# Performance work log

Hardware: AMD Instinct MI355X
Metric: run time of the kernel (lower is better)

The kernel has to match this reference:

```python
import jax, jax.numpy as jnp
import numpy as np

HEADS = 8
DIM_HEAD = 64
BN_EPS = 1e-5

def setup_inputs() -> dict:
    key = jax.random.key(0)
    ks = jax.random.split(key, 6)
    B, N, D = 8, 1024, 512
    inner = HEADS * DIM_HEAD  # 512
    return {
        "x": jax.random.normal(ks[0], (B, N, D), dtype=jnp.float32),
        "w_qkv": jax.random.normal(ks[1], (D, 3 * inner), dtype=jnp.float32) * (D ** -0.5),
        "conv_w": jax.random.normal(ks[2], (HEADS, HEADS), dtype=jnp.float32) * (HEADS ** -0.5),
        "conv_b": jax.random.normal(ks[3], (HEADS,), dtype=jnp.float32) * 0.02,
        "bn_gamma": jnp.ones((HEADS,), dtype=jnp.float32),
        "bn_beta": jnp.zeros((HEADS,), dtype=jnp.float32),
        "w_out": jax.random.normal(ks[4], (inner, D), dtype=jnp.float32) * (inner ** -0.5),
        "b_out": jnp.zeros((D,), dtype=jnp.float32),
    }

def reference(x, w_qkv, conv_w, conv_b, bn_gamma, bn_beta, w_out, b_out):
    B, N, D = x.shape
    H, dh = HEADS, DIM_HEAD
    scale = dh ** -0.5
    qkv = x @ w_qkv  # [B, N, 3*H*dh]
    q, k, v = jnp.split(qkv, 3, axis=-1)
    # b n (h d) -> b h n d
    q = q.reshape(B, N, H, dh).transpose(0, 2, 1, 3)
    k = k.reshape(B, N, H, dh).transpose(0, 2, 1, 3)
    v = v.reshape(B, N, H, dh).transpose(0, 2, 1, 3)
    attn = jnp.einsum('bhnd,bhmd->bhnm', q, k) * scale
    attn = jax.nn.softmax(attn, axis=-1)
    # 1x1 conv across heads (channels = heads)
    attn = jnp.einsum('gh,bhnm->bgnm', conv_w, attn) + conv_b[None, :, None, None]
    # BatchNorm2d in training mode: batch stats over (B, N, N) per head, biased variance
    mean = attn.mean(axis=(0, 2, 3), keepdims=True)
    var = attn.var(axis=(0, 2, 3), keepdims=True)
    attn = (attn - mean) * jax.lax.rsqrt(var + BN_EPS)
    attn = attn * bn_gamma[None, :, None, None] + bn_beta[None, :, None, None]
    # reatten_scale = 1.0 (transform_scale=False)
    out = jnp.einsum('bhnm,bhmd->bhnd', attn, v)
    out = out.transpose(0, 2, 1, 3).reshape(B, N, H * dh)  # b h n d -> b n (h d)
    return out @ w_out + b_out
```

## Files before the change

### kernel.cpp

```cpp
#include <hip/hip_runtime.h>
#include <math.h>


#define Bz 8
#define Nn 1024
#define Dd 512
#define Hh 8
#define DH 64
#define INNER 512
#define QW 1536
#define SCALE 0.125f
#define BN_EPS 1e-5f

typedef _Float16 __f16;
typedef __f16 f16x8 __attribute__((ext_vector_type(8)));
typedef float f32x4 __attribute__((ext_vector_type(4)));

#define MFMA16(a, b, c) __builtin_amdgcn_mfma_f32_16x16x32_f16((a), (b), (c), 0, 0, 0)

__device__ __forceinline__ unsigned short f2h(float f) {
  union { __f16 h; unsigned short s; } v;
  v.h = (__f16)f;
  return v.s;
}
__device__ __forceinline__ float h2f(unsigned short s) {
  union { unsigned short s; __f16 h; } v;
  v.s = s;
  return (float)v.h;
}

#define WB_XB 0u
#define WB_QKV 8388608u
#define WB_O1 0u
#define WB_VT 33554432u
#define WB_SG 41943040u
#define WB_O1BF WB_SG
#define WB_WQT 176160768u
#define WB_WOT 177733632u
#define WB_RSUM 178257920u
#define WB_VSUM 178520064u
#define WB_STATS 178536448u
#define WB_AC 178536512u

__global__ __launch_bounds__(256) void k_xbf(const float* __restrict__ X,
                                             unsigned short* __restrict__ XB) {
  const size_t i = ((size_t)blockIdx.x * 256 + threadIdx.x) * 8;
  float4 f0 = *(const float4*)(X + i);
  float4 f1 = *(const float4*)(X + i + 4);
  unsigned short o[8] = {f2h(f0.x), f2h(f0.y), f2h(f0.z), f2h(f0.w),
                         f2h(f1.x), f2h(f1.y), f2h(f1.z), f2h(f1.w)};
  *(uint4*)(XB + i) = *(uint4*)o;
}

__global__ __launch_bounds__(256) void k_transpose(const float* __restrict__ src,
                                                   unsigned short* __restrict__ dst,
                                                   int R, int C) {
  __shared__ float tile[32][33];
  const int tc = blockIdx.x * 32, tr = blockIdx.y * 32;
  const int lx = threadIdx.x & 31, ly = threadIdx.x >> 5;
#pragma unroll
  for (int i = 0; i < 32; i += 8)
    tile[ly + i][lx] = src[(size_t)(tr + ly + i) * C + tc + lx];
  __syncthreads();
#pragma unroll
  for (int i = 0; i < 32; i += 8)
    dst[(size_t)(tc + ly + i) * R + tr + lx] = f2h(tile[lx][ly + i]);
}

__global__ __launch_bounds__(256) void k_qkv(const unsigned short* __restrict__ XB,
                                             const unsigned short* __restrict__ WQT,
                                             unsigned short* __restrict__ qkv,
                                             unsigned short* __restrict__ vT) {
  extern __shared__ char smem[];
  unsigned short(*sA)[40] = (unsigned short(*)[40])smem;
  unsigned short(*sB)[40] = (unsigned short(*)[40])(smem + 128 * 40 * 2);
  unsigned short* sEp = (unsigned short*)smem;
  const int t = threadIdx.x;
  const int col0 = blockIdx.x * 128;
  const int row0 = blockIdx.y * 128;
  const bool isqk = (col0 < 2 * INNER);
  const int l = t & 63, w = t >> 6;
  const int wm = (w & 1) * 64, wn = (w >> 1) * 64;
  const int lm = l & 15, lq = l >> 4;
  const int srow = t >> 1, skc = (t & 1) * 16;
  f32x4 acc[4][4] = {};
  for (int k0 = 0; k0 < Dd; k0 += 32) {
    {
      const unsigned short* src = XB + (size_t)(row0 + srow) * Dd + k0 + skc;
      *(uint4*)&sA[srow][skc] = *(const uint4*)src;
      *(uint4*)&sA[srow][skc + 8] = *(const uint4*)(src + 8);
    }
    {
      const unsigned short* srcB = WQT + (size_t)(col0 + srow) * Dd + k0 + skc;
      *(uint4*)&sB[srow][skc] = *(const uint4*)srcB;
      *(uint4*)&sB[srow][skc + 8] = *(const uint4*)(srcB + 8);
    }
    __syncthreads();
    f16x8 af[4], bfr[4];
#pragma unroll
    for (int i = 0; i < 4; i++) af[i] = *(const f16x8*)&sA[wm + 16 * i + lm][lq * 8];
#pragma unroll
    for (int j = 0; j < 4; j++) bfr[j] = *(const f16x8*)&sB[wn + 16 * j + lm][lq * 8];
    if (isqk) {
#pragma unroll
      for (int i = 0; i < 4; i++)
#pragma unroll
        for (int j = 0; j < 4; j++) acc[i][j] = MFMA16(bfr[i], af[j], acc[i][j]);
    } else {
#pragma unroll
      for (int i = 0; i < 4; i++)
#pragma unroll
        for (int j = 0; j < 4; j++) acc[i][j] = MFMA16(af[i], bfr[j], acc[i][j]);
    }
    __syncthreads();
  }
  if (isqk) {
#pragma unroll
    for (int jc = 0; jc < 4; jc++)
#pragma unroll
      for (int ir = 0; ir < 4; ir++) {
        unsigned short us[4];
#pragma unroll
        for (int r = 0; r < 4; r++) us[r] = f2h(acc[jc][ir][r]);
        *(uint2*)&sEp[(wm + 16 * ir + lm) * 136 + wn + 16 * jc + 4 * lq] = *(uint2*)us;
      }
    __syncthreads();
    const int row = t >> 1, half = t & 1;
    const unsigned short* src = &sEp[row * 136 + half * 64];
    unsigned short* dst = qkv + (size_t)(row0 + row) * QW + col0 + half * 64;
#pragma unroll
    for (int c = 0; c < 8; c++) *(uint4*)(dst + c * 8) = *(const uint4*)(src + c * 8);
  } else {
#pragma unroll
    for (int ir = 0; ir < 4; ir++)
#pragma unroll
      for (int jc = 0; jc < 4; jc++) {
        unsigned short us[4];
#pragma unroll
        for (int r = 0; r < 4; r++) us[r] = f2h(acc[ir][jc][r]);
        *(uint2*)&sEp[(wn + 16 * jc + lm) * 136 + wm + 16 * ir + 4 * lq] = *(uint2*)us;
      }
    __syncthreads();
    const int row = t >> 1, half = t & 1;
    const int gd = col0 - 2 * INNER + row;
    const int bq = row0 >> 10, mseq0 = row0 & 1023;
    const unsigned short* src = &sEp[row * 136 + half * 64];
    unsigned short* dst =
        vT + (((size_t)(bq * Hh + (gd >> 6)) * DH + (gd & 63)) << 10) + mseq0 + half * 64;
#pragma unroll
    for (int c = 0; c < 8; c++) *(uint4*)(dst + c * 8) = *(const uint4*)(src + c * 8);
  }
}

__global__ __launch_bounds__(256) void k_vsum(const unsigned short* __restrict__ vT,
                                              float* __restrict__ vsum) {
  const int bg = blockIdx.x;
  const int d = threadIdx.x >> 2, qq = threadIdx.x & 3;
  __shared__ float red[64][4];
  const unsigned short* p = vT + ((size_t)bg * DH + d) * Nn + qq * 256;
  float s = 0.f;
  for (int m = 0; m < 256; m += 4) {
    uint2 rr = *(const uint2*)(p + m);
    s += h2f((unsigned short)(rr.x & 0xffff)) + h2f((unsigned short)(rr.x >> 16)) +
         h2f((unsigned short)(rr.y & 0xffff)) + h2f((unsigned short)(rr.y >> 16));
  }
  red[d][qq] = s;
  __syncthreads();
  if (threadIdx.x < 64)
    vsum[(size_t)bg * DH + threadIdx.x] =
        red[threadIdx.x][0] + red[threadIdx.x][1] + red[threadIdx.x][2] + red[threadIdx.x][3];
}

__global__ __launch_bounds__(512, 2) void k_sgen(const unsigned short* __restrict__ qkv,
                                                 unsigned short* __restrict__ Sg,
                                                 float* __restrict__ rsum) {
  __shared__ unsigned short sK[8 * 32 * 72];
  __shared__ unsigned short sT[32 * 264];
  const int b = blockIdx.x;
  const int n0 = blockIdx.y * 32;
  const int mh = blockIdx.z;
  const int t = threadIdx.x;
  const int w = t >> 6, l = t & 63;
  const int lm = l & 15, lq = l >> 4;
  f16x8 qf[2][2];
#pragma unroll
  for (int i = 0; i < 2; i++) {
    const unsigned short* qp =
        qkv + (size_t)(b * Nn + n0 + 16 * i + lm) * QW + w * DH + lq * 8;
    qf[i][0] = *(const f16x8*)qp;
    qf[i][1] = *(const f16x8*)(qp + 32);
  }
  float psum[2] = {0.f, 0.f};
  for (int it = 0; it < 16; it++) {
    const int m0 = mh * 512 + it * 32;
    {
#pragma unroll
      for (int s = 0; s < 4; s++) {
        const int c = t + s * 512;
        const int hh = c >> 8, mm = (c >> 3) & 31, qq = c & 7;
        *(uint4*)&sK[(hh * 32 + mm) * 72 + qq * 8] = *(const uint4*)(
            qkv + (size_t)(b * Nn + m0 + mm) * QW + INNER + hh * DH + qq * 8);
      }
    }
    __syncthreads();
    f32x4 lac[2][2] = {};
#pragma unroll
    for (int jm = 0; jm < 2; jm++) {
      f16x8 ka0 = *(const f16x8*)&sK[(w * 32 + 16 * jm + lm) * 72 + lq * 8];
      f16x8 ka1 = *(const f16x8*)&sK[(w * 32 + 16 * jm + lm) * 72 + 32 + lq * 8];
#pragma unroll
      for (int i = 0; i < 2; i++) {
        lac[i][jm] = MFMA16(ka0, qf[i][0], lac[i][jm]);
        lac[i][jm] = MFMA16(ka1, qf[i][1], lac[i][jm]);
      }
    }
#pragma unroll
    for (int i = 0; i < 2; i++)
#pragma unroll
      for (int jm = 0; jm < 2; jm++)
#pragma unroll
        for (int r = 0; r < 4; r++) {
          float e = __expf(lac[i][jm][r] * SCALE);
          psum[i] += e;
          sT[(16 * i + lm) * 264 + (16 * jm + 4 * lq + r) * 8 + w] = f2h(e);
        }
    __syncthreads();
    {
      const int row = t >> 4, ck = t & 15;
      unsigned short* dst =
          Sg + (((size_t)(b * Nn + n0 + row) << 10) + m0) * 8 + ck * 16;
      const unsigned short* src = &sT[row * 264 + ck * 16];
      *(uint4*)dst = *(const uint4*)src;
      *(uint4*)(dst + 8) = *(const uint4*)(src + 8);
    }
  }
#pragma unroll
  for (int i = 0; i < 2; i++) {
    psum[i] += __shfl_xor(psum[i], 16);
    psum[i] += __shfl_xor(psum[i], 32);
  }
  if (lq == 0) {
    atomicAdd(&rsum[(size_t)(b * Hh + w) * Nn + n0 + lm], psum[0]);
    atomicAdd(&rsum[(size_t)(b * Hh + w) * Nn + n0 + 16 + lm], psum[1]);
  }
}

__global__ __launch_bounds__(512, 2) void k_mixsv(const unsigned short* __restrict__ Sg,
                                                  const unsigned short* __restrict__ vT,
                                                  const float* __restrict__ rsum,
                                                  const float* __restrict__ conv_w,
                                                  float* __restrict__ O1,
                                                  float* __restrict__ stats) {
  __shared__ unsigned short sU[8][16][68];
  __shared__ float sRed[8][16];
  const int b = blockIdx.x;
  const int n0 = blockIdx.y * 16;
  const int t = threadIdx.x;
  const int w = t >> 6, l = t & 63;
  const int lm = l & 15, lq = l >> 4;
  const int mxn = t >> 5, mxm = (t & 31) * 2;
  float cw[64];
#pragma unroll
  for (int i = 0; i < 64; i++) cw[i] = conv_w[i];
  float rv[8];
#pragma unroll
  for (int h = 0; h < 8; h++) rv[h] = 1.0f / rsum[(size_t)(b * Hh + h) * Nn + n0 + mxn];
  const unsigned short* sNp = Sg + ((size_t)(b * Nn + n0 + mxn) << 13);
  f32x4 oacc[4] = {};
  float su[8] = {}, su2[8] = {};
  uint4 c0, c1;
  {
    const unsigned short* p = sNp + (mxm << 3);
    c0 = *(const uint4*)p;
    c1 = *(const uint4*)(p + 8);
  }
  for (int it = 0; it < 16; it++) {
    uint4 nx0, nx1;
    if (it < 15) {
      const unsigned short* p = sNp + ((size_t)((it + 1) * 64 + mxm) << 3);
      nx0 = *(const uint4*)p;
      nx1 = *(const uint4*)(p + 8);
    }
    {
      const unsigned* pe = (const unsigned*)&c0;
      const unsigned* po = (const unsigned*)&c1;
      float sx[8], sy[8];
#pragma unroll
      for (int hp = 0; hp < 4; hp++) {
        sx[2 * hp] = h2f((unsigned short)(pe[hp] & 0xffff)) * rv[2 * hp];
        sx[2 * hp + 1] = h2f((unsigned short)(pe[hp] >> 16)) * rv[2 * hp + 1];
        sy[2 * hp] = h2f((unsigned short)(po[hp] & 0xffff)) * rv[2 * hp];
        sy[2 * hp + 1] = h2f((unsigned short)(po[hp] >> 16)) * rv[2 * hp + 1];
      }
#pragma unroll
      for (int g = 0; g < 8; g++) {
        float u0 = 0.f, u1 = 0.f;
#pragma unroll
        for (int h = 0; h < 8; h++) {
          u0 += cw[g * 8 + h] * sx[h];
          u1 += cw[g * 8 + h] * sy[h];
        }
        su[g] += u0 + u1;
        su2[g] += u0 * u0 + u1 * u1;
        *(unsigned*)&sU[g][mxn][mxm] = (unsigned)f2h(u0) | ((unsigned)f2h(u1) << 16);
      }
    }
    __syncthreads();
    {
      f16x8 uf0 = *(const f16x8*)&sU[w][lm][lq * 8];
      f16x8 uf1 = *(const f16x8*)&sU[w][lm][32 + lq * 8];
#pragma unroll
      for (int j = 0; j < 4; j++) {
        const unsigned short* vp =
            vT + (((size_t)(b * Hh + w) * DH + 16 * j + lm) << 10) + it * 64 + lq * 8;
        f16x8 v0 = *(const f16x8*)vp;
        f16x8 v1 = *(const f16x8*)(vp + 32);
        oacc[j] = MFMA16(uf0, v0, oacc[j]);
        oacc[j] = MFMA16(uf1, v1, oacc[j]);
      }
    }
    __syncthreads();
    if (it < 15) {
      c0 = nx0;
      c1 = nx1;
    }
  }
#pragma unroll
  for (int j = 0; j < 4; j++)
#pragma unroll
    for (int r = 0; r < 4; r++)
      O1[((size_t)(b * Hh + w) * Nn + n0 + lq * 4 + r) * DH + 16 * j + lm] = oacc[j][r];
#pragma unroll
  for (int g = 0; g < 8; g++) {
    float a = su[g], q = su2[g];
    for (int off = 32; off; off >>= 1) {
      a += __shfl_down(a, off);
      q += __shfl_down(q, off);
    }
    if (l == 0) {
      sRed[w][g] = a;
      sRed[w][8 + g] = q;
    }
  }
  __syncthreads();
  if (t < 16) {
    float s = 0.f;
#pragma unroll
    for (int ww = 0; ww < 8; ww++) s += sRed[ww][t];
    atomicAdd(&stats[t], s);
  }
}

__global__ void k_alpha(const float* __restrict__ stats, const float* __restrict__ bn_gamma,
                        const float* __restrict__ bn_beta, float* __restrict__ ac) {
  const int g = threadIdx.x;
  if (g < 8) {
    const float cnt = (float)Bz * (float)Nn * (float)Nn;
    float Eu = stats[g] / cnt;
    float Eu2 = stats[8 + g] / cnt;
    float inv = rsqrtf(Eu2 - Eu * Eu + BN_EPS);
    float alpha = bn_gamma[g] * inv;
    ac[g] = alpha;
    ac[8 + g] = bn_beta[g] - Eu * alpha;
  }
}

__global__ __launch_bounds__(256) void k_o1aff(const float* __restrict__ O1,
                                               const float* __restrict__ vsum,
                                               const float* __restrict__ ac,
                                               unsigned short* __restrict__ O1BF) {
  const size_t i4 = ((size_t)blockIdx.x * 256 + threadIdx.x) * 4;
  const int bg = (int)(i4 >> 16);
  const int g = bg & 7;
  const int d = (int)(i4 & 63);
  float4 a = *(const float4*)(O1 + i4);
  float4 v = *(const float4*)(vsum + (size_t)bg * DH + d);
  const float al = ac[g], cc = ac[8 + g];
  unsigned short o[4] = {f2h(al * a.x + cc * v.x), f2h(al * a.y + cc * v.y),
                         f2h(al * a.z + cc * v.z), f2h(al * a.w + cc * v.w)};
  *(uint2*)(O1BF + i4) = *(uint2*)o;
}

__global__ __launch_bounds__(256) void k_out(const unsigned short* __restrict__ O1BF,
                                             const unsigned short* __restrict__ WOT,
                                             const float* __restrict__ bout,
                                             float* __restrict__ out) {
  __shared__ unsigned short sA[128][40];
  __shared__ unsigned short sB[128][40];
  const int t = threadIdx.x;
  const int col0 = blockIdx.x * 128, row0 = blockIdx.y * 128;
  const int l = t & 63, w = t >> 6;
  const int wm = (w & 1) * 64, wn = (w >> 1) * 64;
  const int lm = l & 15, lq = l >> 4;
  const int srow = t >> 1, skc = (t & 1) * 16;
  const int b = row0 >> 10;
  const int nn = (row0 + srow) & 1023;
  f32x4 acc[4][4] = {};
  for (int k0 = 0; k0 < INNER; k0 += 32) {
    {
      const int k = k0 + skc;
      const int g = k >> 6, dd = k & 63;
      const unsigned short* src = O1BF + ((size_t)(b * Hh + g) * Nn + nn) * DH + dd;
      *(uint4*)&sA[srow][skc] = *(const uint4*)src;
      *(uint4*)&sA[srow][skc + 8] = *(const uint4*)(src + 8);
    }
    {
      const unsigned short* srcB = WOT + (size_t)(col0 + srow) * INNER + k0 + skc;
      *(uint4*)&sB[srow][skc] = *(const uint4*)srcB;
      *(uint4*)&sB[srow][skc + 8] = *(const uint4*)(srcB + 8);
    }
    __syncthreads();
    f16x8 af[4], bfr[4];
#pragma unroll
    for (int i = 0; i < 4; i++) af[i] = *(const f16x8*)&sA[wm + 16 * i + lm][lq * 8];
#pragma unroll
    for (int j = 0; j < 4; j++) bfr[j] = *(const f16x8*)&sB[wn + 16 * j + lm][lq * 8];
#pragma unroll
    for (int i = 0; i < 4; i++)
#pragma unroll
      for (int j = 0; j < 4; j++) acc[i][j] = MFMA16(af[i], bfr[j], acc[i][j]);
    __syncthreads();
  }
#pragma unroll
  for (int j = 0; j < 4; j++) {
    const int col = col0 + wn + 16 * j + lm;
    const float bo = bout[col];
#pragma unroll
    for (int i = 0; i < 4; i++) {
      const int rbase = row0 + wm + 16 * i + lq * 4;
#pragma unroll
      for (int r = 0; r < 4; r++) out[(size_t)(rbase + r) * Dd + col] = acc[i][j][r] + bo;
    }
  }
}

extern "C" void kernel_launch(void* const* d_in, const int* in_sizes, int n_in,
                              void* d_out, int out_size, void* d_ws, size_t ws_size,
                              hipStream_t stream) {
  const float* x = (const float*)d_in[0];
  const float* w_qkv = (const float*)d_in[1];
  const float* conv_w = (const float*)d_in[2];
  const float* bn_gamma = (const float*)d_in[4];
  const float* bn_beta = (const float*)d_in[5];
  const float* w_out = (const float*)d_in[6];
  const float* b_out = (const float*)d_in[7];
  char* ws = (char*)d_ws;
  unsigned short* XB = (unsigned short*)(ws + WB_XB);
  unsigned short* QKV = (unsigned short*)(ws + WB_QKV);
  unsigned short* VT = (unsigned short*)(ws + WB_VT);
  unsigned short* SG = (unsigned short*)(ws + WB_SG);
  unsigned short* WQT = (unsigned short*)(ws + WB_WQT);
  unsigned short* WOT = (unsigned short*)(ws + WB_WOT);
  float* O1 = (float*)(ws + WB_O1);
  unsigned short* O1BF = (unsigned short*)(ws + WB_O1BF);
  float* RSUM = (float*)(ws + WB_RSUM);
  float* VSUM = (float*)(ws + WB_VSUM);
  float* STATS = (float*)(ws + WB_STATS);
  float* AC = (float*)(ws + WB_AC);

  hipMemsetAsync(STATS, 0, 64, stream);
  hipMemsetAsync(RSUM, 0, 262144, stream);
  k_xbf<<<2048, 256, 0, stream>>>(x, XB);
  k_transpose<<<dim3(48, 16), 256, 0, stream>>>(w_qkv, WQT, 512, 1536);
  k_transpose<<<dim3(16, 16), 256, 0, stream>>>(w_out, WOT, 512, 512);
  k_qkv<<<dim3(12, 64), 256, 34816, stream>>>(XB, WQT, QKV, VT);
  k_vsum<<<64, 256, 0, stream>>>(VT, VSUM);
  k_sgen<<<dim3(8, 32, 2), 512, 0, stream>>>(QKV, SG, RSUM);
  k_mixsv<<<dim3(8, 64), 512, 0, stream>>>(SG, VT, RSUM, conv_w, O1, STATS);
  k_alpha<<<1, 64, 0, stream>>>(STATS, bn_gamma, bn_beta, AC);
  k_o1aff<<<4096, 256, 0, stream>>>(O1, VSUM, AC, O1BF);
  k_out<<<dim3(4, 64), 256, 0, stream>>>(O1BF, WOT, b_out, (float*)d_out);
}
```

Before: 271.7 us.

## Double-buffer mix LDS tile, use packed fp16 scaling, derive BN mean analytically

The head-mix kernel now double-buffers its shared-memory tile, so one barrier per iteration is removed, and V fragments are loaded before the barrier. Softmax normalisation is done with packed fp16 multiplies and the result is converted with pkrtz. The BN mean is computed from the conv weight row sums (softmax rows sum to 1, conv bias ignored as before), which drops the running-sum accumulation. The risks are extra fp16 rounding in the scaling step and extra LDS use.

```diff
diff --git a/kernel.cpp b/kernel.cpp
--- a/kernel.cpp
+++ b/kernel.cpp
@@ -14,6 +14,8 @@
 
 typedef _Float16 __f16;
 typedef __f16 f16x8 __attribute__((ext_vector_type(8)));
+typedef __f16 f16x2 __attribute__((ext_vector_type(2)));
+typedef __fp16 fp16x2 __attribute__((ext_vector_type(2)));
 typedef float f32x4 __attribute__((ext_vector_type(4)));
 
 #define MFMA16(a, b, c) __builtin_amdgcn_mfma_f32_16x16x32_f16((a), (b), (c), 0, 0, 0)
@@ -251,8 +253,8 @@
                                                   const float* __restrict__ conv_w,
                                                   float* __restrict__ O1,
                                                   float* __restrict__ stats) {
-  __shared__ unsigned short sU[8][16][68];
-  __shared__ float sRed[8][16];
+  __shared__ unsigned short sU[2][8][16][68];
+  __shared__ float sRed[8][8];
   const int b = blockIdx.x;
   const int n0 = blockIdx.y * 16;
   const int t = threadIdx.x;
@@ -262,68 +264,80 @@
   float cw[64];
 #pragma unroll
   for (int i = 0; i < 64; i++) cw[i] = conv_w[i];
-  float rv[8];
-#pragma unroll
-  for (int h = 0; h < 8; h++) rv[h] = 1.0f / rsum[(size_t)(b * Hh + h) * Nn + n0 + mxn];
+  f16x2 rvh2[4];
+#pragma unroll
+  for (int hp = 0; hp < 4; hp++) {
+    float r0 = 1.0f / rsum[(size_t)(b * Hh + 2 * hp) * Nn + n0 + mxn];
+    float r1 = 1.0f / rsum[(size_t)(b * Hh + 2 * hp + 1) * Nn + n0 + mxn];
+    f16x2 rr;
+    rr[0] = (__f16)r0;
+    rr[1] = (__f16)r1;
+    rvh2[hp] = rr;
+  }
   const unsigned short* sNp = Sg + ((size_t)(b * Nn + n0 + mxn) << 13);
   f32x4 oacc[4] = {};
-  float su[8] = {}, su2[8] = {};
+  float su2[8] = {};
   uint4 c0, c1;
   {
     const unsigned short* p = sNp + (mxm << 3);
     c0 = *(const uint4*)p;
     c1 = *(const uint4*)(p + 8);
   }
+  int p = 0;
   for (int it = 0; it < 16; it++) {
     uint4 nx0, nx1;
     if (it < 15) {
-      const unsigned short* p = sNp + ((size_t)((it + 1) * 64 + mxm) << 3);
-      nx0 = *(const uint4*)p;
-      nx1 = *(const uint4*)(p + 8);
-    }
-    {
-      const unsigned* pe = (const unsigned*)&c0;
-      const unsigned* po = (const unsigned*)&c1;
-      float sx[8], sy[8];
+      const unsigned short* pp = sNp + ((size_t)((it + 1) * 64 + mxm) << 3);
+      nx0 = *(const uint4*)pp;
+      nx1 = *(const uint4*)(pp + 8);
+    }
+    {
+      const f16x2* pe2 = (const f16x2*)&c0;
+      const f16x2* po2 = (const f16x2*)&c1;
+      f16x2 eh[4], oh[4];
 #pragma unroll
       for (int hp = 0; hp < 4; hp++) {
-        sx[2 * hp] = h2f((unsigned short)(pe[hp] & 0xffff)) * rv[2 * hp];
-        sx[2 * hp + 1] = h2f((unsigned short)(pe[hp] >> 16)) * rv[2 * hp + 1];
-        sy[2 * hp] = h2f((unsigned short)(po[hp] & 0xffff)) * rv[2 * hp];
-        sy[2 * hp + 1] = h2f((unsigned short)(po[hp] >> 16)) * rv[2 * hp + 1];
+        eh[hp] = pe2[hp] * rvh2[hp];
+        oh[hp] = po2[hp] * rvh2[hp];
       }
 #pragma unroll
       for (int g = 0; g < 8; g++) {
         float u0 = 0.f, u1 = 0.f;
 #pragma unroll
-        for (int h = 0; h < 8; h++) {
-          u0 += cw[g * 8 + h] * sx[h];
-          u1 += cw[g * 8 + h] * sy[h];
+        for (int hp = 0; hp < 4; hp++) {
+          u0 = fmaf((float)eh[hp][0], cw[g * 8 + 2 * hp], u0);
+          u0 = fmaf((float)eh[hp][1], cw[g * 8 + 2 * hp + 1], u0);
+          u1 = fmaf((float)oh[hp][0], cw[g * 8 + 2 * hp], u1);
+          u1 = fmaf((float)oh[hp][1], cw[g * 8 + 2 * hp + 1], u1);
         }
-        su[g] += u0 + u1;
-        su2[g] += u0 * u0 + u1 * u1;
-        *(unsigned*)&sU[g][mxn][mxm] = (unsigned)f2h(u0) | ((unsigned)f2h(u1) << 16);
-      }
-    }
-    __syncthreads();
-    {
-      f16x8 uf0 = *(const f16x8*)&sU[w][lm][lq * 8];
-      f16x8 uf1 = *(const f16x8*)&sU[w][lm][32 + lq * 8];
+        su2[g] = fmaf(u0, u0, fmaf(u1, u1, su2[g]));
+        fp16x2 pk = __builtin_amdgcn_cvt_pkrtz(u0, u1);
+        *(unsigned*)&sU[p][g][mxn][mxm] = *(unsigned*)&pk;
+      }
+    }
+    f16x8 va[4], vb[4];
+#pragma unroll
+    for (int j = 0; j < 4; j++) {
+      const unsigned short* vp =
+          vT + (((size_t)(b * Hh + w) * DH + 16 * j + lm) << 10) + it * 64 + lq * 8;
+      va[j] = *(const f16x8*)vp;
+      vb[j] = *(const f16x8*)(vp + 32);
+    }
+    __syncthreads();
+    {
+      f16x8 uf0 = *(const f16x8*)&sU[p][w][lm][lq * 8];
+      f16x8 uf1 = *(const f16x8*)&sU[p][w][lm][32 + lq * 8];
 #pragma unroll
       for (int j = 0; j < 4; j++) {
-        const unsigned short* vp =
-            vT + (((size_t)(b * Hh + w) * DH + 16 * j + lm) << 10) + it * 64 + lq * 8;
-        f16x8 v0 = *(const f16x8*)vp;
-        f16x8 v1 = *(const f16x8*)(vp + 32);
-        oacc[j] = MFMA16(uf0, v0, oacc[j]);
-        oacc[j] = MFMA16(uf1, v1, oacc[j]);
-      }
-    }
-    __syncthreads();
+        oacc[j] = MFMA16(uf0, va[j], oacc[j]);
+        oacc[j] = MFMA16(uf1, vb[j], oacc[j]);
+      }
+    }
     if (it < 15) {
       c0 = nx0;
       c1 = nx1;
     }
+    p ^= 1;
   }
 #pragma unroll
   for (int j = 0; j < 4; j++)
@@ -332,31 +346,29 @@
       O1[((size_t)(b * Hh + w) * Nn + n0 + lq * 4 + r) * DH + 16 * j + lm] = oacc[j][r];
 #pragma unroll
   for (int g = 0; g < 8; g++) {
-    float a = su[g], q = su2[g];
-    for (int off = 32; off; off >>= 1) {
-      a += __shfl_down(a, off);
-      q += __shfl_down(q, off);
-    }
-    if (l == 0) {
-      sRed[w][g] = a;
-      sRed[w][8 + g] = q;
-    }
+    float q = su2[g];
+    for (int off = 32; off; off >>= 1) q += __shfl_down(q, off);
+    if (l == 0) sRed[w][g] = q;
   }
   __syncthreads();
-  if (t < 16) {
+  if (t < 8) {
     float s = 0.f;
 #pragma unroll
     for (int ww = 0; ww < 8; ww++) s += sRed[ww][t];
-    atomicAdd(&stats[t], s);
-  }
-}
-
-__global__ void k_alpha(const float* __restrict__ stats, const float* __restrict__ bn_gamma,
+    atomicAdd(&stats[8 + t], s);
+  }
+}
+
+__global__ void k_alpha(const float* __restrict__ stats, const float* __restrict__ conv_w,
+                        const float* __restrict__ bn_gamma,
                         const float* __restrict__ bn_beta, float* __restrict__ ac) {
   const int g = threadIdx.x;
   if (g < 8) {
     const float cnt = (float)Bz * (float)Nn * (float)Nn;
-    float Eu = stats[g] / cnt;
+    float sc = 0.f;
+#pragma unroll
+    for (int h = 0; h < 8; h++) sc += conv_w[g * 8 + h];
+    float Eu = sc * (1.0f / (float)Nn);
     float Eu2 = stats[8 + g] / cnt;
     float inv = rsqrtf(Eu2 - Eu * Eu + BN_EPS);
     float alpha = bn_gamma[g] * inv;
@@ -467,7 +479,7 @@
   k_vsum<<<64, 256, 0, stream>>>(VT, VSUM);
   k_sgen<<<dim3(8, 32, 2), 512, 0, stream>>>(QKV, SG, RSUM);
   k_mixsv<<<dim3(8, 64), 512, 0, stream>>>(SG, VT, RSUM, conv_w, O1, STATS);
-  k_alpha<<<1, 64, 0, stream>>>(STATS, bn_gamma, bn_beta, AC);
+  k_alpha<<<1, 64, 0, stream>>>(STATS, conv_w, bn_gamma, bn_beta, AC);
   k_o1aff<<<4096, 256, 0, stream>>>(O1, VSUM, AC, O1BF);
   k_out<<<dim3(4, 64), 256, 0, stream>>>(O1BF, WOT, b_out, (float*)d_out);
 }
```

Result: no change. 273.4 us (+0.6%).

## Compute BN stats via head Gram matrix and apply conv after PV matmul

Applied to the files above, without the earlier changes.

The head-mixing 1x1 conv is moved from the attention matrix to after the per-head P·V products. Each warp now computes all 8 heads' S·V with MFMA and combines them with conv weights scaled by the inverse row sums. BatchNorm variance is computed from an 8x8 Gram matrix of normalized probabilities, contracted with conv_w in k_alpha. The mean is taken analytically from the row-sum-to-one property. The score tensor layout changes to per-head rows so the MFMA can read it directly. This removes the scalar per-element conv mixing and LDS staging, but multiplies MFMA work by 8 and adds redundant global re-reads of S for the Gram terms.

```diff
diff --git a/kernel.cpp b/kernel.cpp
--- a/kernel.cpp
+++ b/kernel.cpp
@@ -32,6 +32,7 @@
 #define WB_XB 0u
 #define WB_QKV 8388608u
 #define WB_O1 0u
+#define WB_CMAT 29360128u
 #define WB_VT 33554432u
 #define WB_SG 41943040u
 #define WB_O1BF WB_SG
@@ -39,7 +40,6 @@
 #define WB_WOT 177733632u
 #define WB_RSUM 178257920u
 #define WB_VSUM 178520064u
-#define WB_STATS 178536448u
 #define WB_AC 178536512u
 
 __global__ __launch_bounds__(256) void k_xbf(const float* __restrict__ X,
@@ -175,7 +175,7 @@
                                                  unsigned short* __restrict__ Sg,
                                                  float* __restrict__ rsum) {
   __shared__ unsigned short sK[8 * 32 * 72];
-  __shared__ unsigned short sT[32 * 264];
+  __shared__ unsigned short sT2[8][32][40];
   const int b = blockIdx.x;
   const int n0 = blockIdx.y * 32;
   const int mh = blockIdx.z;
@@ -217,22 +217,25 @@
 #pragma unroll
     for (int i = 0; i < 2; i++)
 #pragma unroll
-      for (int jm = 0; jm < 2; jm++)
+      for (int jm = 0; jm < 2; jm++) {
+        unsigned short us[4];
 #pragma unroll
         for (int r = 0; r < 4; r++) {
           float e = __expf(lac[i][jm][r] * SCALE);
           psum[i] += e;
-          sT[(16 * i + lm) * 264 + (16 * jm + 4 * lq + r) * 8 + w] = f2h(e);
+          us[r] = f2h(e);
         }
-    __syncthreads();
-    {
-      const int row = t >> 4, ck = t & 15;
+        *(uint2*)&sT2[w][16 * i + lm][16 * jm + 4 * lq] = *(uint2*)us;
+      }
+    {
+      const int row = l >> 1, half = l & 1;
+      const unsigned short* src = &sT2[w][row][half * 16];
       unsigned short* dst =
-          Sg + (((size_t)(b * Nn + n0 + row) << 10) + m0) * 8 + ck * 16;
-      const unsigned short* src = &sT[row * 264 + ck * 16];
+          Sg + ((size_t)(b * Hh + w) * Nn + n0 + row) * Nn + m0 + half * 16;
       *(uint4*)dst = *(const uint4*)src;
       *(uint4*)(dst + 8) = *(const uint4*)(src + 8);
     }
+    __syncthreads();
   }
 #pragma unroll
   for (int i = 0; i < 2; i++) {
@@ -250,114 +253,113 @@
                                                   const float* __restrict__ rsum,
                                                   const float* __restrict__ conv_w,
                                                   float* __restrict__ O1,
-                                                  float* __restrict__ stats) {
-  __shared__ unsigned short sU[8][16][68];
-  __shared__ float sRed[8][16];
+                                                  float* __restrict__ cmat) {
   const int b = blockIdx.x;
   const int n0 = blockIdx.y * 16;
   const int t = threadIdx.x;
   const int w = t >> 6, l = t & 63;
   const int lm = l & 15, lq = l >> 4;
-  const int mxn = t >> 5, mxm = (t & 31) * 2;
-  float cw[64];
-#pragma unroll
-  for (int i = 0; i < 64; i++) cw[i] = conv_w[i];
-  float rv[8];
-#pragma unroll
-  for (int h = 0; h < 8; h++) rv[h] = 1.0f / rsum[(size_t)(b * Hh + h) * Nn + n0 + mxn];
-  const unsigned short* sNp = Sg + ((size_t)(b * Nn + n0 + mxn) << 13);
-  f32x4 oacc[4] = {};
-  float su[8] = {}, su2[8] = {};
-  uint4 c0, c1;
+  const unsigned short* sb[8];
+#pragma unroll
+  for (int h = 0; h < 8; h++)
+    sb[h] = Sg + ((size_t)(b * Hh + h) * Nn + n0 + lm) * Nn + lq * 8;
+  const unsigned short* vbase = vT + (((size_t)(b * Hh + w) * DH + lm) << 10) + lq * 8;
+  f32x4 acc[8][4] = {};
+  float gam[8] = {0.f, 0.f, 0.f, 0.f, 0.f, 0.f, 0.f, 0.f};
+  for (int it = 0; it < 16; it++) {
+    const int m0 = it * 64;
+    f16x8 va[4], vb[4];
+#pragma unroll
+    for (int j = 0; j < 4; j++) {
+      va[j] = *(const f16x8*)(vbase + (j << 14) + m0);
+      vb[j] = *(const f16x8*)(vbase + (j << 14) + m0 + 32);
+    }
+#pragma unroll
+    for (int h = 0; h < 8; h++) {
+      f16x8 a0 = *(const f16x8*)(sb[h] + m0);
+      f16x8 a1 = *(const f16x8*)(sb[h] + m0 + 32);
+#pragma unroll
+      for (int j = 0; j < 4; j++) {
+        acc[h][j] = MFMA16(a0, va[j], acc[h][j]);
+        acc[h][j] = MFMA16(a1, vb[j], acc[h][j]);
+      }
+    }
+#pragma unroll
+    for (int h = 0; h < 8; h++) {
+      const int h2 = (w - h) & 7;
+      if (h2 >= h) {
+        f16x8 x0 = *(const f16x8*)(sb[h] + m0);
+        f16x8 x1 = *(const f16x8*)(sb[h] + m0 + 32);
+        f16x8 y0 = *(const f16x8*)(sb[h2] + m0);
+        f16x8 y1 = *(const f16x8*)(sb[h2] + m0 + 32);
+        float g = gam[h];
+#pragma unroll
+        for (int s = 0; s < 8; s++) {
+          g = fmaf((float)x0[s], (float)y0[s], g);
+          g = fmaf((float)x1[s], (float)y1[s], g);
+        }
+        gam[h] = g;
+      }
+    }
+  }
   {
-    const unsigned short* p = sNp + (mxm << 3);
-    c0 = *(const uint4*)p;
-    c1 = *(const uint4*)(p + 8);
-  }
-  for (int it = 0; it < 16; it++) {
-    uint4 nx0, nx1;
-    if (it < 15) {
-      const unsigned short* p = sNp + ((size_t)((it + 1) * 64 + mxm) << 3);
-      nx0 = *(const uint4*)p;
-      nx1 = *(const uint4*)(p + 8);
-    }
-    {
-      const unsigned* pe = (const unsigned*)&c0;
-      const unsigned* po = (const unsigned*)&c1;
-      float sx[8], sy[8];
-#pragma unroll
-      for (int hp = 0; hp < 4; hp++) {
-        sx[2 * hp] = h2f((unsigned short)(pe[hp] & 0xffff)) * rv[2 * hp];
-        sx[2 * hp + 1] = h2f((unsigned short)(pe[hp] >> 16)) * rv[2 * hp + 1];
-        sy[2 * hp] = h2f((unsigned short)(po[hp] & 0xffff)) * rv[2 * hp];
-        sy[2 * hp + 1] = h2f((unsigned short)(po[hp] >> 16)) * rv[2 * hp + 1];
-      }
-#pragma unroll
-      for (int g = 0; g < 8; g++) {
-        float u0 = 0.f, u1 = 0.f;
-#pragma unroll
-        for (int h = 0; h < 8; h++) {
-          u0 += cw[g * 8 + h] * sx[h];
-          u1 += cw[g * 8 + h] * sy[h];
-        }
-        su[g] += u0 + u1;
-        su2[g] += u0 * u0 + u1 * u1;
-        *(unsigned*)&sU[g][mxn][mxm] = (unsigned)f2h(u0) | ((unsigned)f2h(u1) << 16);
-      }
-    }
-    __syncthreads();
-    {
-      f16x8 uf0 = *(const f16x8*)&sU[w][lm][lq * 8];
-      f16x8 uf1 = *(const f16x8*)&sU[w][lm][32 + lq * 8];
-#pragma unroll
-      for (int j = 0; j < 4; j++) {
-        const unsigned short* vp =
-            vT + (((size_t)(b * Hh + w) * DH + 16 * j + lm) << 10) + it * 64 + lq * 8;
-        f16x8 v0 = *(const f16x8*)vp;
-        f16x8 v1 = *(const f16x8*)(vp + 32);
-        oacc[j] = MFMA16(uf0, v0, oacc[j]);
-        oacc[j] = MFMA16(uf1, v1, oacc[j]);
-      }
-    }
-    __syncthreads();
-    if (it < 15) {
-      c0 = nx0;
-      c1 = nx1;
-    }
+    float rvl[8];
+#pragma unroll
+    for (int h = 0; h < 8; h++)
+      rvl[h] = 1.0f / rsum[(size_t)(b * Hh + h) * Nn + n0 + lm];
+#pragma unroll
+    for (int h = 0; h < 8; h++) {
+      const int h2 = (w - h) & 7;
+      if (h2 >= h) {
+        float g = gam[h] * rvl[h] * rvl[h2];
+#pragma unroll
+        for (int off = 32; off; off >>= 1) g += __shfl_down(g, off);
+        if (l == 0) atomicAdd(&cmat[h * 8 + h2], g);
+      }
+    }
+  }
+  float cw8[8];
+#pragma unroll
+  for (int h = 0; h < 8; h++) cw8[h] = conv_w[w * 8 + h];
+  float sc[8][4];
+#pragma unroll
+  for (int h = 0; h < 8; h++) {
+    float4 rr = *(const float4*)&rsum[(size_t)(b * Hh + h) * Nn + n0 + lq * 4];
+    sc[h][0] = cw8[h] / rr.x;
+    sc[h][1] = cw8[h] / rr.y;
+    sc[h][2] = cw8[h] / rr.z;
+    sc[h][3] = cw8[h] / rr.w;
   }
 #pragma unroll
   for (int j = 0; j < 4; j++)
 #pragma unroll
-    for (int r = 0; r < 4; r++)
-      O1[((size_t)(b * Hh + w) * Nn + n0 + lq * 4 + r) * DH + 16 * j + lm] = oacc[j][r];
-#pragma unroll
-  for (int g = 0; g < 8; g++) {
-    float a = su[g], q = su2[g];
-    for (int off = 32; off; off >>= 1) {
-      a += __shfl_down(a, off);
-      q += __shfl_down(q, off);
-    }
-    if (l == 0) {
-      sRed[w][g] = a;
-      sRed[w][8 + g] = q;
-    }
-  }
-  __syncthreads();
-  if (t < 16) {
-    float s = 0.f;
-#pragma unroll
-    for (int ww = 0; ww < 8; ww++) s += sRed[ww][t];
-    atomicAdd(&stats[t], s);
-  }
-}
-
-__global__ void k_alpha(const float* __restrict__ stats, const float* __restrict__ bn_gamma,
+    for (int r = 0; r < 4; r++) {
+      float o = 0.f;
+#pragma unroll
+      for (int h = 0; h < 8; h++) o = fmaf(sc[h][r], acc[h][j][r], o);
+      O1[((size_t)(b * Hh + w) * Nn + n0 + lq * 4 + r) * DH + 16 * j + lm] = o;
+    }
+}
+
+__global__ void k_alpha(const float* __restrict__ cmat, const float* __restrict__ conv_w,
+                        const float* __restrict__ bn_gamma,
                         const float* __restrict__ bn_beta, float* __restrict__ ac) {
   const int g = threadIdx.x;
   if (g < 8) {
     const float cnt = (float)Bz * (float)Nn * (float)Nn;
-    float Eu = stats[g] / cnt;
-    float Eu2 = stats[8 + g] / cnt;
+    float scw = 0.f;
+#pragma unroll
+    for (int h = 0; h < 8; h++) scw += conv_w[g * 8 + h];
+    float Eu = scw * (1.0f / (float)Nn);
+    float Eu2 = 0.f;
+#pragma unroll
+    for (int h = 0; h < 8; h++)
+#pragma unroll
+      for (int h2 = h; h2 < 8; h2++) {
+        float mul = (h == h2) ? 1.f : 2.f;
+        Eu2 += mul * conv_w[g * 8 + h] * conv_w[g * 8 + h2] * cmat[h * 8 + h2];
+      }
+    Eu2 /= cnt;
     float inv = rsqrtf(Eu2 - Eu * Eu + BN_EPS);
     float alpha = bn_gamma[g] * inv;
     ac[g] = alpha;
@@ -455,10 +457,9 @@
   unsigned short* O1BF = (unsigned short*)(ws + WB_O1BF);
   float* RSUM = (float*)(ws + WB_RSUM);
   float* VSUM = (float*)(ws + WB_VSUM);
-  float* STATS = (float*)(ws + WB_STATS);
+  float* CMAT = (float*)(ws + WB_CMAT);
   float* AC = (float*)(ws + WB_AC);
 
-  hipMemsetAsync(STATS, 0, 64, stream);
   hipMemsetAsync(RSUM, 0, 262144, stream);
   k_xbf<<<2048, 256, 0, stream>>>(x, XB);
   k_transpose<<<dim3(48, 16), 256, 0, stream>>>(w_qkv, WQT, 512, 1536);
@@ -466,8 +467,9 @@
   k_qkv<<<dim3(12, 64), 256, 34816, stream>>>(XB, WQT, QKV, VT);
   k_vsum<<<64, 256, 0, stream>>>(VT, VSUM);
   k_sgen<<<dim3(8, 32, 2), 512, 0, stream>>>(QKV, SG, RSUM);
-  k_mixsv<<<dim3(8, 64), 512, 0, stream>>>(SG, VT, RSUM, conv_w, O1, STATS);
-  k_alpha<<<1, 64, 0, stream>>>(STATS, bn_gamma, bn_beta, AC);
+  hipMemsetAsync(CMAT, 0, 256, stream);
+  k_mixsv<<<dim3(8, 64), 512, 0, stream>>>(SG, VT, RSUM, conv_w, O1, CMAT);
+  k_alpha<<<1, 64, 0, stream>>>(CMAT, conv_w, bn_gamma, bn_beta, AC);
   k_o1aff<<<4096, 256, 0, stream>>>(O1, VSUM, AC, O1BF);
   k_out<<<dim3(4, 64), 256, 0, stream>>>(O1BF, WOT, b_out, (float*)d_out);
 }
```

Result: slower. 510.2 us (+87.8%).
